# Performance work log

Measured on AMD Instinct MI355X. Metric: run time of the kernel, lower is better.

## Reference

```python
import jax, jax.numpy as jnp
import numpy as np

N = 100000
E = 1600000
D_IN, D_OUT = 25, 50


def _seg_softmax(scores, seg, num_segments):
    m = jax.ops.segment_max(scores, seg, num_segments=num_segments)
    e = jnp.exp(scores - m[seg])
    s = jax.ops.segment_sum(e, seg, num_segments=num_segments)
    return e / (s[seg] + 1e-16)


def gatv2_conv(x, ei, Wl, bl, Wr, br, att, bo):
    # PyG GATv2Conv, heads=1, concat=True, add_self_loops=True, negative_slope=0.2
    n = x.shape[0]
    loops = jnp.arange(n, dtype=ei.dtype)
    src = jnp.concatenate([ei[0], loops])  # message sources j
    dst = jnp.concatenate([ei[1], loops])  # message targets i
    xl = x @ Wl + bl  # [N, 50] source transform
    xr = x @ Wr + br  # [N, 50] target transform
    m = jax.nn.leaky_relu(xl[src] + xr[dst], 0.2)  # [E+N, 50]
    scores = m @ att  # [E+N]
    alpha = _seg_softmax(scores, dst, n)
    out = jax.ops.segment_sum(alpha[:, None] * xl[src], dst, num_segments=n)
    return out + bo


def setup_inputs() -> dict:
    key = jax.random.key(0)
    ks = jax.random.split(key, 32)
    d = {}
    d['x'] = jax.random.normal(ks[0], (N, D_IN), dtype=jnp.float32)
    d['ei_p'] = jax.random.randint(ks[1], (2, E), 0, N, dtype=jnp.int32)
    d['ei_s'] = jax.random.randint(ks[2], (2, E), 0, N, dtype=jnp.int32)
    d['ei_v'] = jax.random.randint(ks[3], (2, E), 0, N, dtype=jnp.int32)
    i = 4
    for tag in ('p', 's', 'v'):
        d['Wl_' + tag] = jax.random.normal(ks[i], (D_IN, D_OUT), dtype=jnp.float32) * 0.2; i += 1
        d['bl_' + tag] = jnp.zeros((D_OUT,), jnp.float32)
        d['Wr_' + tag] = jax.random.normal(ks[i], (D_IN, D_OUT), dtype=jnp.float32) * 0.2; i += 1
        d['br_' + tag] = jnp.zeros((D_OUT,), jnp.float32)
        d['att_' + tag] = jax.random.normal(ks[i], (D_OUT,), dtype=jnp.float32) * 0.2; i += 1
        d['bo_' + tag] = jnp.zeros((D_OUT,), jnp.float32)
    d['proj_W'] = jax.random.normal(ks[i], (150, 150), dtype=jnp.float32) * 0.08; i += 1
    d['proj_b'] = jnp.zeros((150,), jnp.float32)
    d['cls_W1'] = jax.random.normal(ks[i], (150, 75), dtype=jnp.float32) * 0.08; i += 1
    d['cls_b1'] = jnp.zeros((75,), jnp.float32)
    d['cls_W2'] = jax.random.normal(ks[i], (75, 30), dtype=jnp.float32) * 0.12; i += 1
    d['cls_b2'] = jnp.zeros((30,), jnp.float32)
    d['cls_W3'] = jax.random.normal(ks[i], (30, 2), dtype=jnp.float32) * 0.18; i += 1
    d['cls_b3'] = jnp.zeros((2,), jnp.float32)
    return d


def reference(x, ei_p, ei_s, ei_v,
              Wl_p, bl_p, Wr_p, br_p, att_p, bo_p,
              Wl_s, bl_s, Wr_s, br_s, att_s, bo_s,
              Wl_v, bl_v, Wr_v, br_v, att_v, bo_v,
              proj_W, proj_b, cls_W1, cls_b1, cls_W2, cls_b2, cls_W3, cls_b3):
    act = lambda h: jax.nn.leaky_relu(h, 0.1)
    x_p = act(gatv2_conv(x, ei_p, Wl_p, bl_p, Wr_p, br_p, att_p, bo_p))
    x_s = act(gatv2_conv(x, ei_s, Wl_s, bl_s, Wr_s, br_s, att_s, bo_s))
    x_v = act(gatv2_conv(x, ei_v, Wl_v, bl_v, Wr_v, br_v, att_v, bo_v))
    h = jnp.concatenate((x_p, x_s, x_v), axis=1)  # [N, 150]
    h = h @ proj_W + proj_b
    h = act(h @ cls_W1 + cls_b1)
    h = act(h @ cls_W2 + cls_b2)
    return h @ cls_W3 + cls_b3  # [N, 2]
```

## Files before the change

### kernel.cpp

```cpp
#include <hip/hip_runtime.h>
#include <hip/hip_fp16.h>

#define N_NODES 100000
#define N_EDGES 1600000
#define D_IN 25
#define D_OUT 50
#define NBKT_C 391
#define BSTR_C 4800
#define DPB 64
#define NBKT_F 1563
#define EPB 8192
#define NBLK_E 196
#define CAP 1536

typedef __attribute__((ext_vector_type(8))) _Float16 half8;
typedef __attribute__((ext_vector_type(2))) _Float16 h2;
typedef __attribute__((ext_vector_type(4))) float float4v;

__device__ __forceinline__ float lrelu(float x, float a) { return fmaxf(x, a * x); }
__device__ __forceinline__ h2 bch2(unsigned u) { return __builtin_bit_cast(h2, u); }

__global__ __launch_bounds__(256) void bkt_scatter_kernel(
    const int* __restrict__ eip, const int* __restrict__ eis, const int* __restrict__ eiv,
    unsigned* __restrict__ bcur3, unsigned* __restrict__ bucketed3)
{
    int t = blockIdx.y;
    const int* ei = (t == 0) ? eip : ((t == 1) ? eis : eiv);
    unsigned* bcur = bcur3 + t * NBKT_C;
    unsigned* bucketed = bucketed3 + (size_t)t * NBKT_C * BSTR_C;
    __shared__ unsigned h[NBKT_C];
    __shared__ unsigned cur[NBKT_C];
    int tid = threadIdx.x;
    for (int b = tid; b < NBKT_C; b += 256) h[b] = 0;
    __syncthreads();
#pragma unroll
    for (int i = 0; i < EPB / 256; ++i) {
        int e = blockIdx.x * EPB + i * 256 + tid;
        if (e < N_EDGES) atomicAdd(&h[(unsigned)ei[N_EDGES + e] >> 8], 1u);
    }
    __syncthreads();
    for (int b = tid; b < NBKT_C; b += 256)
        cur[b] = (unsigned)b * BSTR_C + (h[b] ? atomicAdd(&bcur[b], h[b]) : 0u);
    __syncthreads();
#pragma unroll
    for (int i = 0; i < EPB / 256; ++i) {
        int e = blockIdx.x * EPB + i * 256 + tid;
        if (e < N_EDGES) {
            unsigned s = (unsigned)ei[e];
            unsigned d = (unsigned)ei[N_EDGES + e];
            unsigned b = d >> 8;
            unsigned r = atomicAdd(&cur[b], 1u);
            if (r < (b + 1u) * BSTR_C)
                bucketed[r] = ((d & 255u) << 17) | s;
        }
    }
}

__device__ __forceinline__ void pack_seg(
    const float* __restrict__ W, unsigned short* __restrict__ outp,
    int K, int O, int NKS, int idx)
{
    int f = idx >> 9, r = idx & 511;
    int l = r >> 3, j = r & 7;
    int ot = f / NKS, ks = f - ot * NKS;
    int k = ks * 32 + (l >> 4) * 8 + j;
    int o = ot * 16 + (l & 15);
    float val = (k < K && o < O) ? W[k * O + o] : 0.f;
    outp[idx] = __half_as_ushort(__float2half_rn(val));
}

__global__ __launch_bounds__(256) void pack_all_kernel(
    const float* __restrict__ projW, const float* __restrict__ W1,
    const float* __restrict__ W2, const float* __restrict__ W3,
    const float* __restrict__ b0, const float* __restrict__ b1,
    const float* __restrict__ b2, const float* __restrict__ b3,
    const float* __restrict__ Wl0, const float* __restrict__ Wr0,
    const float* __restrict__ Wl1, const float* __restrict__ Wr1,
    const float* __restrict__ Wl2, const float* __restrict__ Wr2,
    const float* __restrict__ bl0, const float* __restrict__ br0,
    const float* __restrict__ bl1, const float* __restrict__ br1,
    const float* __restrict__ bl2, const float* __restrict__ br2,
    unsigned short* __restrict__ wpkAll, float* __restrict__ biasPad,
    __half* __restrict__ xl3)
{
    int gid = blockIdx.x * 256 + threadIdx.x;
    if (gid < 25600) pack_seg(projW, wpkAll, 150, 150, 5, gid);
    else if (gid < 40960) pack_seg(W1, wpkAll + 25600, 150, 75, 5, gid - 25600);
    else if (gid < 44032) pack_seg(W2, wpkAll + 40960, 75, 30, 3, gid - 40960);
    else if (gid < 44544) pack_seg(W3, wpkAll + 44032, 30, 2, 1, gid - 44032);
    else if (gid < 56832) {
        int t = gid - 44544;
        int mat = t >> 11, idx = t & 2047;
        const float* Wm = (mat == 0) ? Wl0 : (mat == 1) ? Wr0 : (mat == 2) ? Wl1
                        : (mat == 3) ? Wr1 : (mat == 4) ? Wl2 : Wr2;
        int ot = idx >> 9, r = idx & 511;
        int l = r >> 3, j = r & 7;
        int k = (l >> 4) * 8 + j;
        int o = ot * 16 + (l & 15);
        float val = (k < D_IN && o < D_OUT) ? Wm[k * D_OUT + o] : 0.f;
        wpkAll[44544 + t] = __half_as_ushort(__float2half_rn(val));
    } else if (gid < 57520) {
        int t = gid - 56832;
        float v;
        if (t < 304) {
            if (t < 160) v = (t < 150) ? b0[t] : 0.f;
            else if (t < 256) { int i = t - 160; v = (i < 75) ? b1[i] : 0.f; }
            else if (t < 288) { int i = t - 256; v = (i < 30) ? b2[i] : 0.f; }
            else { int i = t - 288; v = (i < 2) ? b3[i] : 0.f; }
        } else {
            int ii = t - 304;
            int mat = ii >> 6, o = ii & 63;
            const float* bm = (mat == 0) ? bl0 : (mat == 1) ? br0 : (mat == 2) ? bl1
                            : (mat == 3) ? br1 : (mat == 4) ? bl2 : br2;
            v = (o < D_OUT) ? bm[o] : 0.f;
        }
        biasPad[t] = v;
    } else if (gid < 57584) {
        xl3[(size_t)3 * N_NODES * 64 + (gid - 57520)] = __ushort_as_half((unsigned short)0);
    }
}

#define TSTR 32
#define OSTR 72

__global__ __launch_bounds__(256) void transform_mfma_kernel(
    const float* __restrict__ x,
    const unsigned short* __restrict__ wpkAll, const float* __restrict__ biasPad,
    __half* __restrict__ xl3, __half* __restrict__ xr3)
{
    __shared__ _Float16 sX[64 * TSTR];
    __shared__ _Float16 sO[4][16 * OSTR];
    int tid = threadIdx.x;
    int w = tid >> 6, l = tid & 63;
    int g0 = blockIdx.x * 64;
    for (int i = tid; i < 64 * D_IN; i += 256) {
        int r = i / D_IN, c = i - r * D_IN;
        int gr = g0 + r;
        sX[r * TSTR + c] = (gr < N_NODES) ? (_Float16)x[(size_t)gr * D_IN + c] : (_Float16)0.f;
    }
    for (int i = tid; i < 64 * 7; i += 256) {
        int r = i / 7, c = D_IN + (i - r * 7);
        sX[r * TSTR + c] = (_Float16)0.f;
    }
    __syncthreads();
    int lm = l & 15, q = l >> 4;
    half8 a = *(const half8*)(sX + (w * 16 + lm) * TSTR + q * 8);
    const unsigned short* wT = wpkAll + 44544;
#pragma unroll
    for (int mat = 0; mat < 6; ++mat) {
        float4v acc[4];
#pragma unroll
        for (int ot = 0; ot < 4; ++ot) {
            half8 b = *(const half8*)(wT + (mat * 4 + ot) * 512 + l * 8);
            float4v z = {0.f, 0.f, 0.f, 0.f};
            acc[ot] = __builtin_amdgcn_mfma_f32_16x16x32_f16(a, b, z, 0, 0, 0);
        }
#pragma unroll
        for (int ot = 0; ot < 4; ++ot) {
            float bv = biasPad[304 + mat * 64 + ot * 16 + lm];
#pragma unroll
            for (int r = 0; r < 4; ++r)
                sO[w][(q * 4 + r) * OSTR + ot * 16 + lm] = (_Float16)(acc[ot][r] + bv);
        }
        __half* dst = ((mat & 1) ? xr3 : xl3) + (size_t)(mat >> 1) * N_NODES * 64;
#pragma unroll
        for (int it = 0; it < 2; ++it) {
            int idx = it * 64 + l;
            int rr = idx >> 3, cc = idx & 7;
            int gr = g0 + w * 16 + rr;
            if (gr < N_NODES) {
                uint4 v = *(const uint4*)&sO[w][rr * OSTR + cc * 8];
                *(uint4*)&dst[(size_t)gr * 64 + cc * 8] = v;
            }
        }
    }
}

__device__ __forceinline__ float edge_score8(uint4 u, const h2* xr, const h2* at)
{
    const h2 k2 = {(_Float16)0.2f, (_Float16)0.2f};
    float acc = 0.f;
    unsigned uu[4] = {u.x, u.y, u.z, u.w};
#pragma unroll
    for (int i = 0; i < 4; ++i) {
        h2 m = bch2(uu[i]) + xr[i];
        m = __builtin_elementwise_max(m, m * k2);
        acc = __builtin_amdgcn_fdot2(m, at[i], acc, false);
    }
    return acc;
}
__device__ __forceinline__ void accum8(float2* O, float w, uint4 u)
{
    unsigned uu[4] = {u.x, u.y, u.z, u.w};
#pragma unroll
    for (int i = 0; i < 4; ++i) {
        h2 xv = bch2(uu[i]);
        O[i].x += w * (float)xv[0];
        O[i].y += w * (float)xv[1];
    }
}

__global__ __launch_bounds__(256) void bkt_gat_kernel(
    const unsigned* __restrict__ bucketed3, const unsigned* __restrict__ bcur3,
    const __half* __restrict__ xl3, const __half* __restrict__ xr3,
    const float* __restrict__ att0, const float* __restrict__ att1, const float* __restrict__ att2,
    const float* __restrict__ bo0, const float* __restrict__ bo1, const float* __restrict__ bo2,
    __half* __restrict__ h16)
{
    int tag = blockIdx.y, b = blockIdx.x;
    int cb = b >> 2;
    unsigned qd = (unsigned)(b & 3);
    const unsigned* bucketed = bucketed3 + (size_t)tag * NBKT_C * BSTR_C + (size_t)cb * BSTR_C;
    const uint4* xl4 = (const uint4*)xl3 + (size_t)tag * N_NODES * 8;
    const uint4* xr4 = (const uint4*)xr3 + (size_t)tag * N_NODES * 8;
    const float* att = (tag == 0) ? att0 : (tag == 1) ? att1 : att2;
    const float* bo  = (tag == 0) ? bo0  : (tag == 1) ? bo1  : bo2;
    int col0 = tag * 50;

    __shared__ unsigned hist[DPB];
    __shared__ unsigned dstart[DPB + 1];
    __shared__ unsigned cur[DPB];
    __shared__ __align__(16) unsigned srcsL[CAP];
    __shared__ unsigned nextD;
    int tid = threadIdx.x;
    unsigned cnt = bcur3[tag * NBKT_C + cb];
    if (cnt > BSTR_C) cnt = BSTR_C;
    if (tid < DPB) hist[tid] = 0;
    if (tid == 0) nextD = 0;
    __syncthreads();
    for (unsigned i = tid; i < cnt; i += 256) {
        unsigned ld = bucketed[i] >> 17;
        if ((ld >> 6) == qd) atomicAdd(&hist[ld & 63u], 1u);
    }
    __syncthreads();
    unsigned c = 0, pc = 0;
    if (tid < DPB) {
        c = hist[tid];
        pc = (c + 3u) & ~3u;
        hist[tid] = pc;
    }
    __syncthreads();
    for (int off = 1; off < DPB; off <<= 1) {
        unsigned v = (tid >= off && tid < DPB) ? hist[tid - off] : 0;
        __syncthreads();
        if (tid < DPB) hist[tid] += v;
        __syncthreads();
    }
    if (tid < DPB) {
        unsigned excl = hist[tid] - pc;
        dstart[tid] = excl;
        cur[tid] = excl;
        if (tid == DPB - 1) dstart[DPB] = hist[DPB - 1];
    }
    __syncthreads();
    for (unsigned i = tid; i < cnt; i += 256) {
        unsigned w = bucketed[i];
        unsigned ld = w >> 17;
        if ((ld >> 6) == qd) {
            unsigned r = atomicAdd(&cur[ld & 63u], 1u);
            if (r < (unsigned)CAP)
                srcsL[r] = (w & 0x1FFFFu) << 3;
        }
    }
    if (tid < DPB) {
        const unsigned DUMMY = 0x80000000u | ((unsigned)(3 * N_NODES) << 3);
        unsigned excl = dstart[tid];
        for (unsigned k = c; k < pc; ++k) {
            unsigned r = excl + k;
            if (r < (unsigned)CAP) srcsL[r] = DUMMY;
        }
    }
    __syncthreads();

    const int l = tid & 7;
    const int grpBase = tid & ~7;
    int c0 = 8 * l;
    h2 at[4];
#pragma unroll
    for (int i = 0; i < 4; ++i) {
        int cc = c0 + 2 * i;
        float lo = (cc < D_OUT) ? att[cc] : 0.f;
        float hi = (cc + 1 < D_OUT) ? att[cc + 1] : 0.f;
        at[i] = h2{(_Float16)lo, (_Float16)hi};
    }
    for (;;) {
        unsigned d;
        if (l == 0) d = atomicAdd(&nextD, 1u);
        d = (unsigned)__shfl((int)d, grpBase);
        if (d >= (unsigned)DPB) break;
        int g = (cb << 8) + (int)(qd << 6) + (int)d;
        if (g >= N_NODES) continue;
        uint4 xru = xr4[g * 8 + l];
        h2 xr[4] = {bch2(xru.x), bch2(xru.y), bch2(xru.z), bch2(xru.w)};
        uint4 xs = xl4[g * 8 + l];

        float q = edge_score8(xs, xr, at);
        q += __shfl_xor(q, 1); q += __shfl_xor(q, 2); q += __shfl_xor(q, 4);
        float S = __expf(q);
        float2 O[4] = {{0.f, 0.f}, {0.f, 0.f}, {0.f, 0.f}, {0.f, 0.f}};
        accum8(O, S, xs);

        unsigned j = dstart[d], jE = dstart[d + 1];
        if (j < jE) {
            uint4 vv = *(const uint4*)&srcsL[j];
            uint4 c0v = xl4[(vv.x & 0x7FFFFFFFu) + l];
            uint4 c1v = xl4[(vv.y & 0x7FFFFFFFu) + l];
            uint4 c2v = xl4[(vv.z & 0x7FFFFFFFu) + l];
            uint4 c3v = xl4[(vv.w & 0x7FFFFFFFu) + l];
            for (;;) {
                j += 4;
                bool more = j < jE;
                uint4 nv, p0v, p1v, p2v, p3v;
                if (more) {
                    nv = *(const uint4*)&srcsL[j];
                    p0v = xl4[(nv.x & 0x7FFFFFFFu) + l];
                    p1v = xl4[(nv.y & 0x7FFFFFFFu) + l];
                    p2v = xl4[(nv.z & 0x7FFFFFFFu) + l];
                    p3v = xl4[(nv.w & 0x7FFFFFFFu) + l];
                }
                float p0 = edge_score8(c0v, xr, at);
                float p1 = edge_score8(c1v, xr, at);
                float p2 = edge_score8(c2v, xr, at);
                float p3 = edge_score8(c3v, xr, at);
                p0 += __shfl_xor(p0, 1); p0 += __shfl_xor(p0, 2); p0 += __shfl_xor(p0, 4);
                p1 += __shfl_xor(p1, 1); p1 += __shfl_xor(p1, 2); p1 += __shfl_xor(p1, 4);
                p2 += __shfl_xor(p2, 1); p2 += __shfl_xor(p2, 2); p2 += __shfl_xor(p2, 4);
                p3 += __shfl_xor(p3, 1); p3 += __shfl_xor(p3, 2); p3 += __shfl_xor(p3, 4);
                float w0 = (vv.x & 0x80000000u) ? 0.f : __expf(p0);
                float w1 = (vv.y & 0x80000000u) ? 0.f : __expf(p1);
                float w2 = (vv.z & 0x80000000u) ? 0.f : __expf(p2);
                float w3 = (vv.w & 0x80000000u) ? 0.f : __expf(p3);
                S += (w0 + w1) + (w2 + w3);
                accum8(O, w0, c0v);
                accum8(O, w1, c1v);
                accum8(O, w2, c2v);
                accum8(O, w3, c3v);
                if (!more) break;
                vv = nv; c0v = p0v; c1v = p1v; c2v = p2v; c3v = p3v;
            }
        }
        float inv = 1.f / (S + 1e-16f);
        size_t base = (size_t)g * 160 + col0 + c0;
#pragma unroll
        for (int i = 0; i < 4; ++i) {
            int cc = c0 + 2 * i;
            if (cc + 1 < D_OUT) {
                float blo = bo[cc], bhi = bo[cc + 1];
                float vlo = lrelu(O[i].x * inv + blo, 0.1f);
                float vhi = lrelu(O[i].y * inv + bhi, 0.1f);
                *(__half2*)&h16[base + 2 * i] = __floats2half2_rn(vlo, vhi);
            }
        }
    }
}

#define HS 168

template<int NOT, int NKS, bool ACT>
__device__ __forceinline__ void head_layer(
    const _Float16* __restrict__ in, _Float16* __restrict__ outp,
    const unsigned short* __restrict__ wp, const float* __restrict__ bias, int l)
{
    const int lm = l & 15, q = l >> 4;
    const _Float16* aBase = in + lm * HS + q * 8;
#pragma unroll
    for (int ot = 0; ot < NOT; ++ot) {
        float4v acc = {0.f, 0.f, 0.f, 0.f};
        const unsigned short* bBase = wp + (ot * NKS) * 512 + l * 8;
#pragma unroll
        for (int ks = 0; ks < NKS; ++ks) {
            half8 a = *(const half8*)(aBase + ks * 32);
            half8 b = *(const half8*)(bBase + ks * 512);
            acc = __builtin_amdgcn_mfma_f32_16x16x32_f16(a, b, acc, 0, 0, 0);
        }
        float bv = bias[ot * 16 + lm];
#pragma unroll
        for (int r = 0; r < 4; ++r) {
            float v = acc[r] + bv;
            if (ACT) v = lrelu(v, 0.1f);
            outp[(q * 4 + r) * HS + ot * 16 + lm] = (_Float16)v;
        }
    }
}

__global__ __launch_bounds__(256) void mfma_head_kernel(
    const __half* __restrict__ h16,
    const unsigned short* __restrict__ wpkAll, const float* __restrict__ biasPad,
    float* __restrict__ out)
{
    __shared__ _Float16 sIn[4][16 * HS];
    __shared__ _Float16 sOut[4][16 * HS];
    int tid = threadIdx.x;
    int w = tid >> 6, l = tid & 63;
    int g0 = blockIdx.x * 64 + w * 16;

    const uint2* hq = (const uint2*)h16;
    for (int idx = l; idx < 16 * 42; idx += 64) {
        int row = idx / 42, qc = idx - row * 42;
        int gn = g0 + row;
        uint2 u = {0u, 0u};
        if (gn < N_NODES && qc < 40) {
            u = hq[(size_t)gn * 40 + qc];
            if (qc == 37) u.y = 0u;
            else if (qc > 37) { u.x = 0u; u.y = 0u; }
        }
        *(uint2*)&sIn[w][row * HS + qc * 4] = u;
    }
    __syncthreads();
    head_layer<10, 5, false>(sIn[w], sOut[w], wpkAll,         biasPad + 0,   l);
    __syncthreads();
    head_layer<6, 5, true >(sOut[w], sIn[w], wpkAll + 25600,  biasPad + 160, l);
    __syncthreads();
    head_layer<2, 3, true >(sIn[w], sOut[w], wpkAll + 40960,  biasPad + 256, l);
    __syncthreads();
    {
        const int lm = l & 15, q = l >> 4;
        float4v acc = {0.f, 0.f, 0.f, 0.f};
        half8 a = *(const half8*)(sOut[w] + lm * HS + q * 8);
        half8 b = *(const half8*)(wpkAll + 44032 + l * 8);
        acc = __builtin_amdgcn_mfma_f32_16x16x32_f16(a, b, acc, 0, 0, 0);
        if (lm < 2) {
            float bv = biasPad[288 + lm];
#pragma unroll
            for (int r = 0; r < 4; ++r) {
                int node = g0 + q * 4 + r;
                if (node < N_NODES) out[node * 2 + lm] = acc[r] + bv;
            }
        }
    }
}

extern "C" void kernel_launch(void* const* d_in, const int* in_sizes, int n_in,
                              void* d_out, int out_size, void* d_ws, size_t ws_size,
                              hipStream_t stream)
{
    const float* x = (const float*)d_in[0];
    const int* eip = (const int*)d_in[1];
    const int* eis = (const int*)d_in[2];
    const int* eiv = (const int*)d_in[3];
    const float *Wl[3], *bl[3], *Wr[3], *br[3], *att[3], *bo[3];
    for (int t = 0; t < 3; ++t) {
        int b = 4 + t * 6;
        Wl[t] = (const float*)d_in[b + 0];
        bl[t] = (const float*)d_in[b + 1];
        Wr[t] = (const float*)d_in[b + 2];
        br[t] = (const float*)d_in[b + 3];
        att[t] = (const float*)d_in[b + 4];
        bo[t] = (const float*)d_in[b + 5];
    }
    const float* projW = (const float*)d_in[22];
    const float* projb = (const float*)d_in[23];
    const float* W1 = (const float*)d_in[24];
    const float* b1 = (const float*)d_in[25];
    const float* W2 = (const float*)d_in[26];
    const float* b2 = (const float*)d_in[27];
    const float* W3 = (const float*)d_in[28];
    const float* b3 = (const float*)d_in[29];
    float* out = (float*)d_out;

    char* ws = (char*)d_ws;
    size_t off = 0;
    auto alloc = [&](size_t bytes) -> char* {
        char* p = ws + off;
        off += (bytes + 255) & ~(size_t)255;
        return p;
    };
    __half* xl3 = (__half*)alloc(((size_t)3 * N_NODES * 64 + 64) * 2);
    __half* xr3 = (__half*)alloc((size_t)3 * N_NODES * 64 * 2);
    unsigned* bucketed3 = (unsigned*)alloc((size_t)3 * NBKT_C * BSTR_C * 4);
    unsigned* bcur3 = (unsigned*)alloc((size_t)3 * NBKT_C * 4);
    __half* h16 = (__half*)alloc((size_t)N_NODES * 160 * 2);
    unsigned short* wpkAll = (unsigned short*)alloc(56832 * 2);
    float* biasPad = (float*)alloc(688 * 4);

    hipMemsetAsync(bcur3, 0, (size_t)3 * NBKT_C * 4, stream);
    pack_all_kernel<<<226, 256, 0, stream>>>(
        projW, W1, W2, W3, projb, b1, b2, b3,
        Wl[0], Wr[0], Wl[1], Wr[1], Wl[2], Wr[2],
        bl[0], br[0], bl[1], br[1], bl[2], br[2],
        wpkAll, biasPad, xl3);

    bkt_scatter_kernel<<<dim3(NBLK_E, 3), 256, 0, stream>>>(eip, eis, eiv, bcur3, bucketed3);

    transform_mfma_kernel<<<(N_NODES + 63) / 64, 256, 0, stream>>>(
        x, wpkAll, biasPad, xl3, xr3);

    bkt_gat_kernel<<<dim3(NBKT_F, 3), 256, 0, stream>>>(
        bucketed3, bcur3, xl3, xr3,
        att[0], att[1], att[2], bo[0], bo[1], bo[2], h16);

    mfma_head_kernel<<<(N_NODES + 63) / 64, 256, 0, stream>>>(h16, wpkAll, biasPad, out);
}
```

Measured before the change: 401.6 us.

## Split per-destination sort into separate kernel and vectorize edge scatter loads

Adds a bkt_sort_kernel that sorts each coarse bucket by local destination once and writes a padded CSR-like source list plus dstart offsets to global memory. The GAT kernel then reads these directly instead of each of four quarter-blocks rescanning the whole coarse bucket and building its own shared-memory list. This removes redundant scans and shrinks the GAT kernel's shared memory footprint, at the cost of an extra launch and an extra global write and read of the sorted lists. The scatter kernel also loads edge indices as int4.

Measured after the change: 390.2 us. 1.03x faster.

```diff
diff --git a/kernel.cpp b/kernel.cpp
--- a/kernel.cpp
+++ b/kernel.cpp
@@ -7,11 +7,11 @@
 #define D_OUT 50
 #define NBKT_C 391
 #define BSTR_C 4800
+#define BSTR_S 5568
 #define DPB 64
 #define NBKT_F 1563
 #define EPB 8192
 #define NBLK_E 196
-#define CAP 1536
 
 typedef __attribute__((ext_vector_type(8))) _Float16 half8;
 typedef __attribute__((ext_vector_type(2))) _Float16 h2;
@@ -22,38 +22,98 @@
 
 __global__ __launch_bounds__(256) void bkt_scatter_kernel(
     const int* __restrict__ eip, const int* __restrict__ eis, const int* __restrict__ eiv,
-    unsigned* __restrict__ bcur3, unsigned* __restrict__ bucketed3)
+    unsigned* __restrict__ bcur3, unsigned* __restrict__ bucketedC)
 {
     int t = blockIdx.y;
     const int* ei = (t == 0) ? eip : ((t == 1) ? eis : eiv);
     unsigned* bcur = bcur3 + t * NBKT_C;
-    unsigned* bucketed = bucketed3 + (size_t)t * NBKT_C * BSTR_C;
+    unsigned* bucketed = bucketedC + (size_t)t * NBKT_C * BSTR_C;
     __shared__ unsigned h[NBKT_C];
     __shared__ unsigned cur[NBKT_C];
     int tid = threadIdx.x;
     for (int b = tid; b < NBKT_C; b += 256) h[b] = 0;
     __syncthreads();
 #pragma unroll
-    for (int i = 0; i < EPB / 256; ++i) {
-        int e = blockIdx.x * EPB + i * 256 + tid;
-        if (e < N_EDGES) atomicAdd(&h[(unsigned)ei[N_EDGES + e] >> 8], 1u);
+    for (int i = 0; i < EPB / 1024; ++i) {
+        int e = blockIdx.x * EPB + (i * 256 + tid) * 4;
+        if (e < N_EDGES) {
+            int4 d4 = *(const int4*)&ei[N_EDGES + e];
+            atomicAdd(&h[(unsigned)d4.x >> 8], 1u);
+            atomicAdd(&h[(unsigned)d4.y >> 8], 1u);
+            atomicAdd(&h[(unsigned)d4.z >> 8], 1u);
+            atomicAdd(&h[(unsigned)d4.w >> 8], 1u);
+        }
     }
     __syncthreads();
     for (int b = tid; b < NBKT_C; b += 256)
         cur[b] = (unsigned)b * BSTR_C + (h[b] ? atomicAdd(&bcur[b], h[b]) : 0u);
     __syncthreads();
 #pragma unroll
-    for (int i = 0; i < EPB / 256; ++i) {
-        int e = blockIdx.x * EPB + i * 256 + tid;
+    for (int i = 0; i < EPB / 1024; ++i) {
+        int e = blockIdx.x * EPB + (i * 256 + tid) * 4;
         if (e < N_EDGES) {
-            unsigned s = (unsigned)ei[e];
-            unsigned d = (unsigned)ei[N_EDGES + e];
-            unsigned b = d >> 8;
-            unsigned r = atomicAdd(&cur[b], 1u);
-            if (r < (b + 1u) * BSTR_C)
-                bucketed[r] = ((d & 255u) << 17) | s;
-        }
-    }
+            int4 s4 = *(const int4*)&ei[e];
+            int4 d4 = *(const int4*)&ei[N_EDGES + e];
+            int ss[4] = {s4.x, s4.y, s4.z, s4.w};
+            int dd[4] = {d4.x, d4.y, d4.z, d4.w};
+#pragma unroll
+            for (int k = 0; k < 4; ++k) {
+                unsigned d = (unsigned)dd[k];
+                unsigned b = d >> 8;
+                unsigned r = atomicAdd(&cur[b], 1u);
+                if (r < (b + 1u) * BSTR_C)
+                    bucketed[r] = ((d & 255u) << 17) | (unsigned)ss[k];
+            }
+        }
+    }
+}
+
+__global__ __launch_bounds__(256) void bkt_sort_kernel(
+    const unsigned* __restrict__ bucketedC, const unsigned* __restrict__ bcur3,
+    unsigned* __restrict__ srcsS, unsigned* __restrict__ dstartAll)
+{
+    int tag = blockIdx.y, cb = blockIdx.x;
+    const unsigned* in = bucketedC + ((size_t)tag * NBKT_C + cb) * BSTR_C;
+    unsigned* outp = srcsS + (size_t)tag * NBKT_C * BSTR_S + (size_t)cb * BSTR_S;
+    unsigned* dstart = dstartAll + ((size_t)tag * NBKT_C + cb) * 257;
+    __shared__ unsigned hist[256];
+    __shared__ unsigned cur[256];
+    __shared__ __align__(16) unsigned sbuf[BSTR_S];
+    __shared__ unsigned totS;
+    int tid = threadIdx.x;
+    unsigned cnt = bcur3[tag * NBKT_C + cb];
+    if (cnt > BSTR_C) cnt = BSTR_C;
+    hist[tid] = 0;
+    __syncthreads();
+    for (unsigned i = tid; i < cnt; i += 256) atomicAdd(&hist[in[i] >> 17], 1u);
+    __syncthreads();
+    unsigned c = hist[tid];
+    unsigned pc = (c + 3u) & ~3u;
+    hist[tid] = pc;
+    __syncthreads();
+    for (int off = 1; off < 256; off <<= 1) {
+        unsigned v = (tid >= off) ? hist[tid - off] : 0u;
+        __syncthreads();
+        hist[tid] += v;
+        __syncthreads();
+    }
+    unsigned excl = hist[tid] - pc;
+    cur[tid] = excl;
+    dstart[tid] = (unsigned)cb * BSTR_S + excl;
+    if (tid == 255) { dstart[256] = (unsigned)cb * BSTR_S + hist[255]; totS = hist[255]; }
+    __syncthreads();
+    for (unsigned i = tid; i < cnt; i += 256) {
+        unsigned w = in[i];
+        unsigned r = atomicAdd(&cur[w >> 17], 1u);
+        sbuf[r] = (w & 0x1FFFFu) << 3;
+    }
+    {
+        const unsigned DUMMY = 0x80000000u | ((unsigned)(3 * N_NODES) << 3);
+        for (unsigned k = c; k < pc; ++k) sbuf[excl + k] = DUMMY;
+    }
+    __syncthreads();
+    unsigned tot = totS;
+    for (unsigned i = tid; i < tot; i += 256) outp[i] = sbuf[i];
 }
 
 __device__ __forceinline__ void pack_seg(
@@ -201,75 +261,26 @@
 }
 
 __global__ __launch_bounds__(256) void bkt_gat_kernel(
-    const unsigned* __restrict__ bucketed3, const unsigned* __restrict__ bcur3,
+    const unsigned* __restrict__ srcsS, const unsigned* __restrict__ dstartAll,
     const __half* __restrict__ xl3, const __half* __restrict__ xr3,
     const float* __restrict__ att0, const float* __restrict__ att1, const float* __restrict__ att2,
     const float* __restrict__ bo0, const float* __restrict__ bo1, const float* __restrict__ bo2,
     __half* __restrict__ h16)
 {
-    int tag = blockIdx.y, b = blockIdx.x;
-    int cb = b >> 2;
-    unsigned qd = (unsigned)(b & 3);
-    const unsigned* bucketed = bucketed3 + (size_t)tag * NBKT_C * BSTR_C + (size_t)cb * BSTR_C;
+    int tag = blockIdx.y, fb = blockIdx.x;
+    int cb = fb >> 2;
+    int qd = fb & 3;
+    const unsigned* srcs = srcsS + (size_t)tag * NBKT_C * BSTR_S;
+    const unsigned* dstart = dstartAll + ((size_t)tag * NBKT_C + cb) * 257 + qd * 64;
     const uint4* xl4 = (const uint4*)xl3 + (size_t)tag * N_NODES * 8;
     const uint4* xr4 = (const uint4*)xr3 + (size_t)tag * N_NODES * 8;
     const float* att = (tag == 0) ? att0 : (tag == 1) ? att1 : att2;
     const float* bo  = (tag == 0) ? bo0  : (tag == 1) ? bo1  : bo2;
     int col0 = tag * 50;
 
-    __shared__ unsigned hist[DPB];
-    __shared__ unsigned dstart[DPB + 1];
-    __shared__ unsigned cur[DPB];
-    __shared__ __align__(16) unsigned srcsL[CAP];
     __shared__ unsigned nextD;
     int tid = threadIdx.x;
-    unsigned cnt = bcur3[tag * NBKT_C + cb];
-    if (cnt > BSTR_C) cnt = BSTR_C;
-    if (tid < DPB) hist[tid] = 0;
     if (tid == 0) nextD = 0;
-    __syncthreads();
-    for (unsigned i = tid; i < cnt; i += 256) {
-        unsigned ld = bucketed[i] >> 17;
-        if ((ld >> 6) == qd) atomicAdd(&hist[ld & 63u], 1u);
-    }
-    __syncthreads();
-    unsigned c = 0, pc = 0;
-    if (tid < DPB) {
-        c = hist[tid];
-        pc = (c + 3u) & ~3u;
-        hist[tid] = pc;
-    }
-    __syncthreads();
-    for (int off = 1; off < DPB; off <<= 1) {
-        unsigned v = (tid >= off && tid < DPB) ? hist[tid - off] : 0;
-        __syncthreads();
-        if (tid < DPB) hist[tid] += v;
-        __syncthreads();
-    }
-    if (tid < DPB) {
-        unsigned excl = hist[tid] - pc;
-        dstart[tid] = excl;
-        cur[tid] = excl;
-        if (tid == DPB - 1) dstart[DPB] = hist[DPB - 1];
-    }
-    __syncthreads();
-    for (unsigned i = tid; i < cnt; i += 256) {
-        unsigned w = bucketed[i];
-        unsigned ld = w >> 17;
-        if ((ld >> 6) == qd) {
-            unsigned r = atomicAdd(&cur[ld & 63u], 1u);
-            if (r < (unsigned)CAP)
-                srcsL[r] = (w & 0x1FFFFu) << 3;
-        }
-    }
-    if (tid < DPB) {
-        const unsigned DUMMY = 0x80000000u | ((unsigned)(3 * N_NODES) << 3);
-        unsigned excl = dstart[tid];
-        for (unsigned k = c; k < pc; ++k) {
-            unsigned r = excl + k;
-            if (r < (unsigned)CAP) srcsL[r] = DUMMY;
-        }
-    }
     __syncthreads();
 
     const int l = tid & 7;
@@ -288,7 +299,7 @@
         if (l == 0) d = atomicAdd(&nextD, 1u);
         d = (unsigned)__shfl((int)d, grpBase);
         if (d >= (unsigned)DPB) break;
-        int g = (cb << 8) + (int)(qd << 6) + (int)d;
+        int g = (cb << 8) + (qd << 6) + (int)d;
         if (g >= N_NODES) continue;
         uint4 xru = xr4[g * 8 + l];
         h2 xr[4] = {bch2(xru.x), bch2(xru.y), bch2(xru.z), bch2(xru.w)};
@@ -302,7 +313,7 @@
 
         unsigned j = dstart[d], jE = dstart[d + 1];
         if (j < jE) {
-            uint4 vv = *(const uint4*)&srcsL[j];
+            uint4 vv = *(const uint4*)&srcs[j];
             uint4 c0v = xl4[(vv.x & 0x7FFFFFFFu) + l];
             uint4 c1v = xl4[(vv.y & 0x7FFFFFFFu) + l];
             uint4 c2v = xl4[(vv.z & 0x7FFFFFFFu) + l];
@@ -312,7 +323,7 @@
                 bool more = j < jE;
                 uint4 nv, p0v, p1v, p2v, p3v;
                 if (more) {
-                    nv = *(const uint4*)&srcsL[j];
+                    nv = *(const uint4*)&srcs[j];
                     p0v = xl4[(nv.x & 0x7FFFFFFFu) + l];
                     p1v = xl4[(nv.y & 0x7FFFFFFFu) + l];
                     p2v = xl4[(nv.z & 0x7FFFFFFFu) + l];
@@ -467,8 +478,10 @@
     };
     __half* xl3 = (__half*)alloc(((size_t)3 * N_NODES * 64 + 64) * 2);
     __half* xr3 = (__half*)alloc((size_t)3 * N_NODES * 64 * 2);
-    unsigned* bucketed3 = (unsigned*)alloc((size_t)3 * NBKT_C * BSTR_C * 4);
+    unsigned* bucketedC = (unsigned*)alloc((size_t)3 * NBKT_C * BSTR_C * 4);
     unsigned* bcur3 = (unsigned*)alloc((size_t)3 * NBKT_C * 4);
+    unsigned* srcsS = (unsigned*)alloc((size_t)3 * NBKT_C * BSTR_S * 4);
+    unsigned* dstartAll = (unsigned*)alloc((size_t)3 * NBKT_C * 257 * 4);
     __half* h16 = (__half*)alloc((size_t)N_NODES * 160 * 2);
     unsigned short* wpkAll = (unsigned short*)alloc(56832 * 2);
     float* biasPad = (float*)alloc(688 * 4);
@@ -480,13 +493,15 @@
         bl[0], br[0], bl[1], br[1], bl[2], br[2],
         wpkAll, biasPad, xl3);
 
-    bkt_scatter_kernel<<<dim3(NBLK_E, 3), 256, 0, stream>>>(eip, eis, eiv, bcur3, bucketed3);
+    bkt_scatter_kernel<<<dim3(NBLK_E, 3), 256, 0, stream>>>(eip, eis, eiv, bcur3, bucketedC);
+
+    bkt_sort_kernel<<<dim3(NBKT_C, 3), 256, 0, stream>>>(bucketedC, bcur3, srcsS, dstartAll);
 
     transform_mfma_kernel<<<(N_NODES + 63) / 64, 256, 0, stream>>>(
         x, wpkAll, biasPad, xl3, xr3);
 
     bkt_gat_kernel<<<dim3(NBKT_F, 3), 256, 0, stream>>>(
-        bucketed3, bcur3, xl3, xr3,
+        srcsS, dstartAll, xl3, xr3,
         att[0], att[1], att[2], bo[0], bo[1], bo[2], h16);
 
     mfma_head_kernel<<<(N_NODES + 63) / 64, 256, 0, stream>>>(h16, wpkAll, biasPad, out);
```
